# Kernel optimization log

Hardware: AMD Instinct MI355X
Metric: run time of the kernel (lower is better)

The kernel has to match this reference:

```python
import jax, jax.numpy as jnp
import numpy as np

BATCH = 64
FEAT = 2048          # backbone.out_features (ResNet-50)
C = 112              # bottleneck_dim = number of concepts
E = 512              # concept_emb_dim
NUM_CLASSES = 345


def setup_inputs() -> dict:
    key = jax.random.key(0)
    ks = jax.random.split(key, 7)
    s_emb = 1.0 / np.sqrt(FEAT)
    s_p = 1.0 / np.sqrt(2 * E)
    s_h = 1.0 / np.sqrt(C * E)
    return {
        "x": jax.random.normal(ks[0], (BATCH, FEAT), jnp.float32),
        "W_emb": jax.random.normal(ks[1], (C, FEAT, 2 * E), jnp.float32) * s_emb,
        "b_emb": jax.random.normal(ks[2], (C, 2 * E), jnp.float32) * s_emb,
        "W_pint": jax.random.normal(ks[3], (C, 2 * E), jnp.float32) * s_p,
        "b_pint": jax.random.normal(ks[4], (C,), jnp.float32) * s_p,
        "W_head": jax.random.normal(ks[5], (C * E, NUM_CLASSES), jnp.float32) * s_h,
        "b_head": jax.random.normal(ks[6], (NUM_CLASSES,), jnp.float32) * s_h,
    }


def reference(x, W_emb, b_emb, W_pint, b_pint, W_head, b_head):
    # Batched version of the per-concept Linear loop: [B,C,2E]
    embeddings = jnp.einsum("bf,cfe->bce", x, W_emb) + b_emb
    positive_embs = embeddings[..., :E]   # [B,C,E]
    negative_embs = embeddings[..., E:]   # [B,C,E]
    # Per-concept Linear(2E, 1) -> [B,C]
    p_int_logits = jnp.einsum("bce,ce->bc", embeddings, W_pint) + b_pint
    p_int_pos = jax.nn.sigmoid(p_int_logits)              # [B,C]
    p = p_int_pos[..., None]
    mixed_embs = p * positive_embs + (1.0 - p) * negative_embs  # [B,C,E]
    flattened = mixed_embs.reshape(mixed_embs.shape[0], -1)     # [B, C*E]
    final_preds = flattened @ W_head + b_head                   # [B, num_classes]
    return (final_preds, flattened, p_int_pos)
```

## Files before the change

kernel.cpp:

```cpp
#include <hip/hip_runtime.h>

typedef __attribute__((ext_vector_type(4))) float  f4;
typedef __attribute__((ext_vector_type(8))) short  bf16x8;
typedef __attribute__((ext_vector_type(4))) float  f32x4;
typedef __attribute__((ext_vector_type(4))) unsigned short us4;
typedef __attribute__((ext_vector_type(2))) unsigned int u32x2;

#define BATCH 64
#define FEAT 2048
#define NC_C 112
#define TE 1024
#define EE 512
#define NCLS 345
#define NCLSP 352
#define KHEAD 57344

__device__ __forceinline__ unsigned short f2bf(float f) {
    unsigned u = __float_as_uint(f);
    unsigned r = (u + 0x7FFFu + ((u >> 16) & 1u)) >> 16;
    return (unsigned short)r;
}
__device__ __forceinline__ float bf2f(unsigned short h) {
    return __uint_as_float(((unsigned)h) << 16);
}

__global__ __launch_bounds__(256) void k_emb(
    const float* __restrict__ x, const float* __restrict__ W_emb,
    const float* __restrict__ b_emb, unsigned short* __restrict__ emb_bf)
{
    __shared__ __align__(16) unsigned short Alds[64 * 40];
    __shared__ __align__(16) unsigned short Blds[128 * 40];

    const int tid = threadIdx.x;
    const int c  = blockIdx.x >> 3;
    const int n0 = (blockIdx.x & 7) * 128;
    const float* __restrict__ Wc = W_emb + (size_t)c * (FEAT * TE);

    const int w = tid >> 6, l = tid & 63;
    const int mbase = (w & 1) * 32, nbase = (w >> 1) * 64;

    const int a_row = tid >> 3;
    const int a_k4  = (tid & 7) * 4;
    const int b_kp  = tid >> 4;
    const int b_n4  = (tid & 15) * 4;

    f4 a0, a1, pA0, pB0, pA1, pB1;
    {
        const float* ax = x + (size_t)a_row * FEAT + a_k4;
        a0 = *(const f4*)ax;
        a1 = *(const f4*)(ax + 32 * FEAT);
        const float* bp = Wc + (size_t)(2 * b_kp) * TE + n0 + b_n4;
        pA0 = *(const f4*)bp;           pB0 = *(const f4*)(bp + TE);
        pA1 = *(const f4*)(bp + 64);    pB1 = *(const f4*)(bp + TE + 64);
    }

    f32x4 acc[2][4];
#pragma unroll
    for (int i = 0; i < 2; ++i)
#pragma unroll
        for (int j = 0; j < 4; ++j) acc[i][j] = (f32x4){0.f, 0.f, 0.f, 0.f};

    for (int s = 0; s < 64; ++s) {
        __syncthreads();
        {
            u32x2 v0, v1;
            v0[0] = (unsigned)f2bf(a0[0]) | ((unsigned)f2bf(a0[1]) << 16);
            v0[1] = (unsigned)f2bf(a0[2]) | ((unsigned)f2bf(a0[3]) << 16);
            v1[0] = (unsigned)f2bf(a1[0]) | ((unsigned)f2bf(a1[1]) << 16);
            v1[1] = (unsigned)f2bf(a1[2]) | ((unsigned)f2bf(a1[3]) << 16);
            *(u32x2*)&Alds[a_row * 40 + a_k4] = v0;
            *(u32x2*)&Alds[(a_row + 32) * 40 + a_k4] = v1;
        }
        {
            const int koct = b_kp >> 2;
            const int klo  = (2 * b_kp) & 7;
#pragma unroll
            for (int i = 0; i < 4; ++i) {
                int n = b_n4 + i;
                unsigned v = (unsigned)f2bf(pA0[i]) | ((unsigned)f2bf(pB0[i]) << 16);
                *(unsigned*)&Blds[n * 40 + (((koct ^ ((n >> 2) & 3)) << 3) | klo)] = v;
                n += 64;
                unsigned v2 = (unsigned)f2bf(pA1[i]) | ((unsigned)f2bf(pB1[i]) << 16);
                *(unsigned*)&Blds[n * 40 + (((koct ^ ((n >> 2) & 3)) << 3) | klo)] = v2;
            }
        }
        __syncthreads();

        if (s < 63) {
            const int k0 = (s + 1) * 32;
            const float* ax = x + (size_t)a_row * FEAT + k0 + a_k4;
            a0 = *(const f4*)ax;
            a1 = *(const f4*)(ax + 32 * FEAT);
            const float* bp = Wc + (size_t)(k0 + 2 * b_kp) * TE + n0 + b_n4;
            pA0 = *(const f4*)bp;           pB0 = *(const f4*)(bp + TE);
            pA1 = *(const f4*)(bp + 64);    pB1 = *(const f4*)(bp + TE + 64);
        }

        bf16x8 af[2], bfr[4];
#pragma unroll
        for (int si = 0; si < 2; ++si)
            af[si] = *(const bf16x8*)&Alds[(mbase + si * 16 + (l & 15)) * 40 + (l >> 4) * 8];
#pragma unroll
        for (int nf = 0; nf < 4; ++nf) {
            int n = nbase + nf * 16 + (l & 15);
            bfr[nf] = *(const bf16x8*)&Blds[n * 40 + (((l >> 4) ^ ((n >> 2) & 3)) << 3)];
        }
#pragma unroll
        for (int si = 0; si < 2; ++si)
#pragma unroll
            for (int nf = 0; nf < 4; ++nf)
                acc[si][nf] = __builtin_amdgcn_mfma_f32_16x16x32_bf16(
                    af[si], bfr[nf], acc[si][nf], 0, 0, 0);
    }

#pragma unroll
    for (int si = 0; si < 2; ++si)
#pragma unroll
        for (int nf = 0; nf < 4; ++nf) {
            const int nl = nbase + nf * 16 + (l & 15);
            const int ng = n0 + nl;
            const float bias = b_emb[c * TE + ng];
#pragma unroll
            for (int r = 0; r < 4; ++r) {
                const int bb = mbase + si * 16 + (l >> 4) * 4 + r;
                const float v = acc[si][nf][r] + bias;
                emb_bf[((size_t)bb * NC_C + c) * TE + ng] = f2bf(v);
            }
        }
}

__global__ __launch_bounds__(256) void k_mix(
    const unsigned short* __restrict__ emb_bf, const float* __restrict__ W_pint,
    const float* __restrict__ b_pint, float* __restrict__ flat_out,
    float* __restrict__ p_out)
{
    const int tid = threadIdx.x;
    const int l = tid & 63, w = tid >> 6;
    const int pidx = blockIdx.x * 4 + w;
    const int b = pidx / NC_C, c = pidx - b * NC_C;

    const unsigned short* __restrict__ row = emb_bf + ((size_t)b * NC_C + c) * TE;
    const float* __restrict__ wp = W_pint + c * TE;

    float vals[16];
    float dot = 0.f;
#pragma unroll
    for (int i = 0; i < 4; ++i) {
        const int e = 4 * l + 256 * i;
        us4 u = *(const us4*)&row[e];
        f4  wv = *(const f4*)&wp[e];
#pragma unroll
        for (int j = 0; j < 4; ++j) {
            float f = bf2f(u[j]);
            vals[i * 4 + j] = f;
            dot += f * wv[j];
        }
    }
#pragma unroll
    for (int m = 32; m >= 1; m >>= 1) dot += __shfl_xor(dot, m);
    const float logit = dot + b_pint[c];
    const float p = 1.f / (1.f + __expf(-logit));
    if (l == 0) p_out[b * NC_C + c] = p;

    float* __restrict__ fo = flat_out + (size_t)b * KHEAD + c * EE;
#pragma unroll
    for (int i = 0; i < 2; ++i) {
        const int e = 4 * l + 256 * i;
        f4 m;
#pragma unroll
        for (int j = 0; j < 4; ++j)
            m[j] = p * vals[i * 4 + j] + (1.f - p) * vals[(i + 2) * 4 + j];
        *(f4*)&fo[e] = m;
    }
}

__global__ __launch_bounds__(256) void k_init(
    const float* __restrict__ b_head, float* __restrict__ final_out)
{
    const int i = blockIdx.x * 256 + threadIdx.x;
    if (i < BATCH * NCLS) final_out[i] = b_head[i % NCLS];
}

__global__ __launch_bounds__(256) void k_head(
    const float* __restrict__ flat, const float* __restrict__ W_head,
    float* __restrict__ final_out)
{
    __shared__ __align__(16) unsigned short Blds[NCLSP * 40];

    const int tid = threadIdx.x;
    const int w = tid >> 6, l = tid & 63;
    const int k0 = blockIdx.x * 256;

    f32x4 acc[22];
#pragma unroll
    for (int i = 0; i < 22; ++i) acc[i] = (f32x4){0.f, 0.f, 0.f, 0.f};

    for (int s = 0; s < 8; ++s) {
        const int kb = k0 + s * 32;
        __syncthreads();
        for (int idx = tid; idx < 32 * NCLSP; idx += 256) {
            const int k = idx / NCLSP;
            const int n = idx - k * NCLSP;
            const float v = (n < NCLS) ? W_head[(size_t)(kb + k) * NCLS + n] : 0.f;
            Blds[n * 40 + ((((k >> 3) ^ ((n >> 2) & 3)) << 3) | (k & 7))] = f2bf(v);
        }
        __syncthreads();

        const float* __restrict__ ap =
            flat + (size_t)(w * 16 + (l & 15)) * KHEAD + kb + (l >> 4) * 8;
        f4 af0 = *(const f4*)ap;
        f4 af1 = *(const f4*)(ap + 4);
        bf16x8 a;
        a[0] = (short)f2bf(af0[0]); a[1] = (short)f2bf(af0[1]);
        a[2] = (short)f2bf(af0[2]); a[3] = (short)f2bf(af0[3]);
        a[4] = (short)f2bf(af1[0]); a[5] = (short)f2bf(af1[1]);
        a[6] = (short)f2bf(af1[2]); a[7] = (short)f2bf(af1[3]);

#pragma unroll
        for (int nf = 0; nf < 22; ++nf) {
            const int n = nf * 16 + (l & 15);
            bf16x8 bfr = *(const bf16x8*)&Blds[n * 40 + (((l >> 4) ^ ((n >> 2) & 3)) << 3)];
            acc[nf] = __builtin_amdgcn_mfma_f32_16x16x32_bf16(a, bfr, acc[nf], 0, 0, 0);
        }
    }

#pragma unroll
    for (int nf = 0; nf < 22; ++nf) {
        const int n = nf * 16 + (l & 15);
        if (n < NCLS) {
#pragma unroll
            for (int r = 0; r < 4; ++r) {
                const int row = w * 16 + (l >> 4) * 4 + r;
                atomicAdd(&final_out[row * NCLS + n], acc[nf][r]);
            }
        }
    }
}

extern "C" void kernel_launch(void* const* d_in, const int* in_sizes, int n_in,
                              void* d_out, int out_size, void* d_ws, size_t ws_size,
                              hipStream_t stream) {
    const float* x      = (const float*)d_in[0];
    const float* W_emb  = (const float*)d_in[1];
    const float* b_emb  = (const float*)d_in[2];
    const float* W_pint = (const float*)d_in[3];
    const float* b_pint = (const float*)d_in[4];
    const float* W_head = (const float*)d_in[5];
    const float* b_head = (const float*)d_in[6];

    float* out   = (float*)d_out;
    float* final_out = out;
    float* flat  = out + BATCH * NCLS;
    float* p_out = out + BATCH * NCLS + BATCH * KHEAD;

    unsigned short* emb_bf = (unsigned short*)d_ws;

    k_init<<<(BATCH * NCLS + 255) / 256, 256, 0, stream>>>(b_head, final_out);
    k_emb<<<NC_C * 8, 256, 0, stream>>>(x, W_emb, b_emb, emb_bf);
    k_mix<<<(BATCH * NC_C) / 4, 256, 0, stream>>>(emb_bf, W_pint, b_pint, flat, p_out);
    k_head<<<KHEAD / 256, 256, 0, stream>>>(flat, W_head, final_out);
}
```

Measured before the change: 416.4 us.

## Double-buffer emb loads, use packed bf16 convert, replace head atomics with split-K reduce

The embedding GEMM now keeps two register sets of prefetched tiles so global loads run two k-steps ahead of the MFMA work. Manual bf16 rounding is replaced by the hardware v_cvt_pk_bf16_f32 instruction in both GEMMs. The head GEMM drops float atomics and a separate bias-init kernel: it writes per-block partial sums to workspace and a new reduce kernel sums them and adds the bias. This raises register pressure in k_emb and adds workspace traffic plus an extra launch, while making the head result deterministic.

```diff
diff --git a/kernel.cpp b/kernel.cpp
--- a/kernel.cpp
+++ b/kernel.cpp
@@ -23,6 +23,11 @@
 __device__ __forceinline__ float bf2f(unsigned short h) {
     return __uint_as_float(((unsigned)h) << 16);
 }
+__device__ __forceinline__ unsigned cvtpk(float a, float b) {
+    unsigned r;
+    asm("v_cvt_pk_bf16_f32 %0, %1, %2" : "=v"(r) : "v"(a), "v"(b));
+    return r;
+}
 
 __global__ __launch_bounds__(256) void k_emb(
     const float* __restrict__ x, const float* __restrict__ W_emb,
@@ -44,15 +49,38 @@
     const int b_kp  = tid >> 4;
     const int b_n4  = (tid & 15) * 4;
 
-    f4 a0, a1, pA0, pB0, pA1, pB1;
-    {
-        const float* ax = x + (size_t)a_row * FEAT + a_k4;
-        a0 = *(const f4*)ax;
-        a1 = *(const f4*)(ax + 32 * FEAT);
-        const float* bp = Wc + (size_t)(2 * b_kp) * TE + n0 + b_n4;
-        pA0 = *(const f4*)bp;           pB0 = *(const f4*)(bp + TE);
-        pA1 = *(const f4*)(bp + 64);    pB1 = *(const f4*)(bp + TE + 64);
-    }
+    const float* __restrict__ axp = x + (size_t)a_row * FEAT + a_k4;
+    const float* __restrict__ bpp = Wc + (size_t)(2 * b_kp) * TE + n0 + b_n4;
+
+    unsigned short* __restrict__ aw0 = &Alds[a_row * 40 + a_k4];
+    unsigned short* __restrict__ aw1 = &Alds[(a_row + 32) * 40 + a_k4];
+    const int koct = b_kp >> 2, klo = (2 * b_kp) & 7;
+
+    auto ke_load = [&](f4& A0, f4& A1, f4& B0, f4& B1, f4& B2, f4& B3, int kstep) {
+        const float* ax_ = axp + kstep * 32;
+        A0 = *(const f4*)ax_;
+        A1 = *(const f4*)(ax_ + 32 * FEAT);
+        const float* bp_ = bpp + (size_t)kstep * 32 * TE;
+        B0 = *(const f4*)bp_;         B1 = *(const f4*)(bp_ + TE);
+        B2 = *(const f4*)(bp_ + 64);  B3 = *(const f4*)(bp_ + TE + 64);
+    };
+    auto ke_write = [&](const f4& A0, const f4& A1, const f4& B0, const f4& B1,
+                        const f4& B2, const f4& B3) {
+        u32x2 v0, v1;
+        v0[0] = cvtpk(A0[0], A0[1]); v0[1] = cvtpk(A0[2], A0[3]);
+        v1[0] = cvtpk(A1[0], A1[1]); v1[1] = cvtpk(A1[2], A1[3]);
+        *(u32x2*)aw0 = v0;
+        *(u32x2*)aw1 = v1;
+#pragma unroll
+        for (int i = 0; i < 4; ++i) {
+            int n = b_n4 + i;
+            *(unsigned*)&Blds[n * 40 + (((koct ^ ((n >> 2) & 3)) << 3) | klo)] =
+                cvtpk(B0[i], B1[i]);
+            n += 64;
+            *(unsigned*)&Blds[n * 40 + (((koct ^ ((n >> 2) & 3)) << 3) | klo)] =
+                cvtpk(B2[i], B3[i]);
+        }
+    };
 
     f32x4 acc[2][4];
 #pragma unroll
@@ -60,42 +88,7 @@
 #pragma unroll
         for (int j = 0; j < 4; ++j) acc[i][j] = (f32x4){0.f, 0.f, 0.f, 0.f};
 
-    for (int s = 0; s < 64; ++s) {
-        __syncthreads();
-        {
-            u32x2 v0, v1;
-            v0[0] = (unsigned)f2bf(a0[0]) | ((unsigned)f2bf(a0[1]) << 16);
-            v0[1] = (unsigned)f2bf(a0[2]) | ((unsigned)f2bf(a0[3]) << 16);
-            v1[0] = (unsigned)f2bf(a1[0]) | ((unsigned)f2bf(a1[1]) << 16);
-            v1[1] = (unsigned)f2bf(a1[2]) | ((unsigned)f2bf(a1[3]) << 16);
-            *(u32x2*)&Alds[a_row * 40 + a_k4] = v0;
-            *(u32x2*)&Alds[(a_row + 32) * 40 + a_k4] = v1;
-        }
-        {
-            const int koct = b_kp >> 2;
-            const int klo  = (2 * b_kp) & 7;
-#pragma unroll
-            for (int i = 0; i < 4; ++i) {
-                int n = b_n4 + i;
-                unsigned v = (unsigned)f2bf(pA0[i]) | ((unsigned)f2bf(pB0[i]) << 16);
-                *(unsigned*)&Blds[n * 40 + (((koct ^ ((n >> 2) & 3)) << 3) | klo)] = v;
-                n += 64;
-                unsigned v2 = (unsigned)f2bf(pA1[i]) | ((unsigned)f2bf(pB1[i]) << 16);
-                *(unsigned*)&Blds[n * 40 + (((koct ^ ((n >> 2) & 3)) << 3) | klo)] = v2;
-            }
-        }
-        __syncthreads();
-
-        if (s < 63) {
-            const int k0 = (s + 1) * 32;
-            const float* ax = x + (size_t)a_row * FEAT + k0 + a_k4;
-            a0 = *(const f4*)ax;
-            a1 = *(const f4*)(ax + 32 * FEAT);
-            const float* bp = Wc + (size_t)(k0 + 2 * b_kp) * TE + n0 + b_n4;
-            pA0 = *(const f4*)bp;           pB0 = *(const f4*)(bp + TE);
-            pA1 = *(const f4*)(bp + 64);    pB1 = *(const f4*)(bp + TE + 64);
-        }
-
+    auto ke_mfma = [&]() {
         bf16x8 af[2], bfr[4];
 #pragma unroll
         for (int si = 0; si < 2; ++si)
@@ -111,6 +104,25 @@
             for (int nf = 0; nf < 4; ++nf)
                 acc[si][nf] = __builtin_amdgcn_mfma_f32_16x16x32_bf16(
                     af[si], bfr[nf], acc[si][nf], 0, 0, 0);
+    };
+
+    f4 aA0, aA1, bA0, bA1, bA2, bA3;
+    f4 aB0, aB1, bB0, bB1, bB2, bB3;
+    ke_load(aA0, aA1, bA0, bA1, bA2, bA3, 0);
+    ke_load(aB0, aB1, bB0, bB1, bB2, bB3, 1);
+
+    for (int s = 0; s < 64; s += 2) {
+        __syncthreads();
+        ke_write(aA0, aA1, bA0, bA1, bA2, bA3);
+        __syncthreads();
+        if (s < 62) ke_load(aA0, aA1, bA0, bA1, bA2, bA3, s + 2);
+        ke_mfma();
+
+        __syncthreads();
+        ke_write(aB0, aB1, bB0, bB1, bB2, bB3);
+        __syncthreads();
+        if (s < 61) ke_load(aB0, aB1, bB0, bB1, bB2, bB3, s + 3);
+        ke_mfma();
     }
 
 #pragma unroll
@@ -174,28 +186,21 @@
     }
 }
 
-__global__ __launch_bounds__(256) void k_init(
-    const float* __restrict__ b_head, float* __restrict__ final_out)
-{
-    const int i = blockIdx.x * 256 + threadIdx.x;
-    if (i < BATCH * NCLS) final_out[i] = b_head[i % NCLS];
-}
-
 __global__ __launch_bounds__(256) void k_head(
     const float* __restrict__ flat, const float* __restrict__ W_head,
-    float* __restrict__ final_out)
+    float* __restrict__ pbuf, int nsteps)
 {
     __shared__ __align__(16) unsigned short Blds[NCLSP * 40];
 
     const int tid = threadIdx.x;
     const int w = tid >> 6, l = tid & 63;
-    const int k0 = blockIdx.x * 256;
+    const int k0 = blockIdx.x * (nsteps * 32);
 
     f32x4 acc[22];
 #pragma unroll
     for (int i = 0; i < 22; ++i) acc[i] = (f32x4){0.f, 0.f, 0.f, 0.f};
 
-    for (int s = 0; s < 8; ++s) {
+    for (int s = 0; s < nsteps; ++s) {
         const int kb = k0 + s * 32;
         __syncthreads();
         for (int idx = tid; idx < 32 * NCLSP; idx += 256) {
@@ -211,10 +216,12 @@
         f4 af0 = *(const f4*)ap;
         f4 af1 = *(const f4*)(ap + 4);
         bf16x8 a;
-        a[0] = (short)f2bf(af0[0]); a[1] = (short)f2bf(af0[1]);
-        a[2] = (short)f2bf(af0[2]); a[3] = (short)f2bf(af0[3]);
-        a[4] = (short)f2bf(af1[0]); a[5] = (short)f2bf(af1[1]);
-        a[6] = (short)f2bf(af1[2]); a[7] = (short)f2bf(af1[3]);
+        unsigned p0 = cvtpk(af0[0], af0[1]), p1 = cvtpk(af0[2], af0[3]);
+        unsigned p2 = cvtpk(af1[0], af1[1]), p3 = cvtpk(af1[2], af1[3]);
+        a[0] = (short)(p0 & 0xFFFF); a[1] = (short)(p0 >> 16);
+        a[2] = (short)(p1 & 0xFFFF); a[3] = (short)(p1 >> 16);
+        a[4] = (short)(p2 & 0xFFFF); a[5] = (short)(p2 >> 16);
+        a[6] = (short)(p3 & 0xFFFF); a[7] = (short)(p3 >> 16);
 
 #pragma unroll
         for (int nf = 0; nf < 22; ++nf) {
@@ -224,17 +231,29 @@
         }
     }
 
+    float* __restrict__ pb = pbuf + (size_t)blockIdx.x * (64 * NCLSP);
 #pragma unroll
     for (int nf = 0; nf < 22; ++nf) {
         const int n = nf * 16 + (l & 15);
-        if (n < NCLS) {
-#pragma unroll
-            for (int r = 0; r < 4; ++r) {
-                const int row = w * 16 + (l >> 4) * 4 + r;
-                atomicAdd(&final_out[row * NCLS + n], acc[nf][r]);
-            }
-        }
-    }
+#pragma unroll
+        for (int r = 0; r < 4; ++r) {
+            const int row = w * 16 + (l >> 4) * 4 + r;
+            pb[row * NCLSP + n] = acc[nf][r];
+        }
+    }
+}
+
+__global__ __launch_bounds__(256) void k_reduce(
+    const float* __restrict__ pbuf, const float* __restrict__ b_head,
+    float* __restrict__ final_out, int nb)
+{
+    const int i = blockIdx.x * 256 + threadIdx.x;
+    if (i >= BATCH * NCLS) return;
+    const int m = i / NCLS, n = i - m * NCLS;
+    float s = b_head[n];
+    for (int p = 0; p < nb; ++p)
+        s += pbuf[((size_t)p * 64 + m) * NCLSP + n];
+    final_out[i] = s;
 }
 
 extern "C" void kernel_launch(void* const* d_in, const int* in_sizes, int n_in,
@@ -248,15 +267,21 @@
     const float* W_head = (const float*)d_in[5];
     const float* b_head = (const float*)d_in[6];
 
-    float* out   = (float*)d_out;
+    float* out       = (float*)d_out;
     float* final_out = out;
-    float* flat  = out + BATCH * NCLS;
-    float* p_out = out + BATCH * NCLS + BATCH * KHEAD;
+    float* flat      = out + BATCH * NCLS;
+    float* p_out     = out + BATCH * NCLS + BATCH * KHEAD;
 
     unsigned short* emb_bf = (unsigned short*)d_ws;
-
-    k_init<<<(BATCH * NCLS + 255) / 256, 256, 0, stream>>>(b_head, final_out);
+    float* pbuf = (float*)d_ws;
+
+    int NB, nsteps;
+    const size_t need224 = (size_t)224 * 64 * NCLSP * sizeof(float);
+    if (ws_size >= need224) { NB = 224; nsteps = 8; }
+    else                    { NB = 128; nsteps = 14; }
+
     k_emb<<<NC_C * 8, 256, 0, stream>>>(x, W_emb, b_emb, emb_bf);
     k_mix<<<(BATCH * NC_C) / 4, 256, 0, stream>>>(emb_bf, W_pint, b_pint, flat, p_out);
-    k_head<<<KHEAD / 256, 256, 0, stream>>>(flat, W_head, final_out);
-}
+    k_head<<<NB, 256, 0, stream>>>(flat, W_head, pbuf, nsteps);
+    k_reduce<<<(BATCH * NCLS + 255) / 256, 256, 0, stream>>>(pbuf, b_head, final_out, NB);
+}
```

Measured after the change: 432.5 us. 3.9% more time.
